# Kernel optimization log

Hardware: AMD Instinct MI355X
Metric: run time of the kernel (lower is better)

## Reference

```python
import jax, jax.numpy as jnp
import numpy as np
import math

D_MODEL = 1024
N_HEAD = 16


def setup_inputs() -> dict:
    key = jax.random.key(0)
    k1, k2, k3 = jax.random.split(key, 3)
    B, S, E = 2, 2048, D_MODEL
    x = jax.random.normal(k1, (B, S, E), dtype=jnp.float32)
    # Linear weights stored as (in, out); init scaled like typical transformer init
    w_attn = jax.random.normal(k2, (E, 3 * E), dtype=jnp.float32) * (1.0 / math.sqrt(E))
    w_proj = jax.random.normal(k3, (E, E), dtype=jnp.float32) * (1.0 / math.sqrt(E))
    return {"x": x, "w_attn": w_attn, "w_proj": w_proj}


def reference(x, w_attn, w_proj):
    B, S, E = x.shape
    H = N_HEAD
    Dh = E // H
    qkv = x @ w_attn  # (B, S, 3E)
    q, k, v = jnp.split(qkv, 3, axis=-1)
    # (B, H, S, Dh)
    q = q.reshape(B, S, H, Dh).transpose(0, 2, 1, 3)
    k = k.reshape(B, S, H, Dh).transpose(0, 2, 1, 3)
    v = v.reshape(B, S, H, Dh).transpose(0, 2, 1, 3)
    scale = 1.0 / math.sqrt(Dh)
    att = jnp.einsum('bhqd,bhkd->bhqk', q, k) * scale  # (B, H, S, S)
    causal = jnp.tril(jnp.ones((S, S), dtype=bool))
    att = jnp.where(causal, att, -jnp.inf)
    att = jax.nn.softmax(att, axis=-1)
    # dropout = 0.0 (eval mode) -> identity
    y = jnp.einsum('bhqk,bhkd->bhqd', att, v)  # (B, H, S, Dh)
    y = y.transpose(0, 2, 1, 3).reshape(B, S, E)
    return y @ w_proj
```

## Files before the change

kernel.cpp:

```cpp
#include <hip/hip_runtime.h>
#include <hip/hip_bf16.h>

#define S_LEN 2048
#define EMB   1024
#define NH    16
#define DH    64
#define QKV_LD 3072

typedef __attribute__((ext_vector_type(8)))  __bf16 bf16x8;
typedef __attribute__((ext_vector_type(4)))  __bf16 bf16x4;
typedef __attribute__((ext_vector_type(4)))  float  f32x4;
typedef __attribute__((ext_vector_type(16))) float  f32x16;
typedef __attribute__((ext_vector_type(2)))  unsigned int u32x2;

__device__ __forceinline__ void gl_lds16(const void* g, void* l) {
  __builtin_amdgcn_global_load_lds(
      (const __attribute__((address_space(1))) void*)g,
      (__attribute__((address_space(3))) void*)l,
      16, 0, 0);
}

__global__ __launch_bounds__(256)
void prep_fused(const float* __restrict__ x, __bf16* __restrict__ xb,
                const float* __restrict__ w_attn, __bf16* __restrict__ wat,
                const float* __restrict__ w_proj, __bf16* __restrict__ wpt,
                int n8) {
  __shared__ float T[64][65];
  const int bid = blockIdx.x;
  const int tid = threadIdx.x;

  if (bid < 2048) {
    int i = bid * 256 + tid;
    if (i >= n8) return;
    const f32x4* p = (const f32x4*)(x + (size_t)i * 8);
    f32x4 a = p[0], b = p[1];
    bf16x8 o;
    #pragma unroll
    for (int j = 0; j < 4; j++) { o[j] = (__bf16)a[j]; o[4 + j] = (__bf16)b[j]; }
    *(bf16x8*)(xb + (size_t)i * 8) = o;
    return;
  }

  const float* W; __bf16* Wt; int K, N, k0, n0;
  if (bid < 2048 + 768) {
    int t = bid - 2048;
    W = w_attn; Wt = wat; K = 1024; N = 3072;
    n0 = (t % 48) * 64; k0 = (t / 48) * 64;
  } else {
    int t = bid - 2816;
    W = w_proj; Wt = wpt; K = 1024; N = 1024;
    n0 = (t & 15) * 64; k0 = (t >> 4) * 64;
  }
  #pragma unroll
  for (int t = 0; t < 16; t++) {
    int idx = tid + t * 256;
    int r = idx >> 6, c = idx & 63;
    T[r][c] = W[(size_t)(k0 + r) * N + n0 + c];
  }
  __syncthreads();
  #pragma unroll
  for (int t = 0; t < 16; t++) {
    int idx = tid + t * 256;
    int r = idx >> 6, c = idx & 63;
    Wt[(size_t)(n0 + r) * K + k0 + c] = (__bf16)T[c][r];
  }
}

#define TM 128
#define TK 32

template <typename OutT, int TNv>
__global__ __launch_bounds__(256, 2)
void gemm_bf16_mfma(const __bf16* __restrict__ A, const __bf16* __restrict__ Bt,
                    OutT* __restrict__ C, int M, int N, int K) {
  __shared__ __align__(16) __bf16 As[2][TM][TK];
  __shared__ __align__(16) __bf16 Bs[2][TNv][TK];
  const int tid  = threadIdx.x;
  const int lane = tid & 63;
  const int w    = tid >> 6;
  const int wr   = w >> 1, wc = w & 1;
  const int brow = blockIdx.y * TM;
  const int bcol = blockIdx.x * TNv;
  const int l15  = lane & 15;
  const int grp  = lane >> 4;

  constexpr int NBI = TNv / 64;
  constexpr int WCT = TNv / 2;
  constexpr int NN  = WCT / 16;

  auto stage = [&](int k0, int buf) {
    #pragma unroll
    for (int j = 0; j < 2; j++) {
      const int cid = w * 128 + j * 64 + lane;
      const int row = cid >> 2, k8 = (cid & 3) * 8;
      gl_lds16(A + (size_t)(brow + row) * K + k0 + k8,
               &As[buf][0][0] + (size_t)(w * 128 + j * 64) * 8);
    }
    #pragma unroll
    for (int j = 0; j < NBI; j++) {
      const int cid = (w * NBI + j) * 64 + lane;
      const int row = cid >> 2, k8 = (cid & 3) * 8;
      gl_lds16(Bt + (size_t)(bcol + row) * K + k0 + k8,
               &Bs[buf][0][0] + (size_t)((w * NBI + j) * 64) * 8);
    }
  };

  f32x4 acc[4][NN];
  #pragma unroll
  for (int m = 0; m < 4; m++)
    #pragma unroll
    for (int n = 0; n < NN; n++) acc[m][n] = (f32x4){0.f, 0.f, 0.f, 0.f};

  stage(0, 0);
  __syncthreads();

  const int nk = K / TK;
  for (int kt = 0; kt < nk; kt++) {
    const int cur = kt & 1;
    if (kt + 1 < nk) stage((kt + 1) * TK, cur ^ 1);

    bf16x8 a[4], b[NN];
    #pragma unroll
    for (int m = 0; m < 4; m++)
      a[m] = *(const bf16x8*)&As[cur][wr * 64 + m * 16 + l15][grp * 8];
    #pragma unroll
    for (int n = 0; n < NN; n++)
      b[n] = *(const bf16x8*)&Bs[cur][wc * WCT + n * 16 + l15][grp * 8];
    #pragma unroll
    for (int m = 0; m < 4; m++)
      #pragma unroll
      for (int n = 0; n < NN; n++)
        acc[m][n] = __builtin_amdgcn_mfma_f32_16x16x32_bf16(a[m], b[n], acc[m][n], 0, 0, 0);

    __syncthreads();
  }

  #pragma unroll
  for (int m = 0; m < 4; m++)
    #pragma unroll
    for (int r = 0; r < 4; r++) {
      const size_t row = (size_t)(brow + wr * 64 + m * 16 + grp * 4 + r);
      #pragma unroll
      for (int n = 0; n < NN; n++)
        C[row * N + bcol + wc * WCT + n * 16 + l15] = (OutT)acc[m][n][r];
    }
}

#define QB 64
#define KB 64
#define QSCALE 0.18033688f

__device__ __constant__ unsigned char ITEMS[44] = {
  76, 72, 68, 64,
  125, 127, 121, 60,
  123, 117, 119, 113, 56,
  115, 109, 111, 105, 52,
  107, 101, 103, 97, 48,
  99, 93, 95, 89, 44,
  91, 85, 87, 81, 40,
  83, 36,
  32, 28, 24, 20, 16, 12, 8, 4, 0
};

__global__ __launch_bounds__(256, 4)
void attn_mfma(const __bf16* __restrict__ qkv, __bf16* __restrict__ y,
               float* __restrict__ pO, float* __restrict__ pml) {
  __shared__ __align__(16) __bf16 Ks[3][KB][64];
  __shared__ __align__(16) __bf16 Vs[3][4096];

  const int tid  = threadIdx.x;
  const int lane = tid & 63;
  const int w    = tid >> 6;

  const int bid = blockIdx.x;
  const int xcd = bid & 7;
  const int j   = bid >> 3;
  const int g   = xcd * 4 + j / 44;
  const int idx = j % 44;

  const int code  = ITEMS[idx];
  const bool split = code & 1;
  const int khalf = (code >> 1) & 1;
  const int qtile = code >> 2;

  int it0, it1;
  bool diag;
  if (!split) {
    it0 = 0; it1 = qtile + 1; diag = true;
  } else {
    const int half = (qtile + 2) >> 1;
    it0 = khalf ? half : 0;
    it1 = khalf ? qtile + 1 : half;
    diag = (khalf == 1);
  }
  const int h = g & 15, b = g >> 4;
  const int pidx = split ? ((g * 12 + (qtile - 20)) * 2 + khalf) : 0;

  const __bf16* base = qkv + (size_t)b * S_LEN * QKV_LD;

  const int l31 = lane & 31;
  const int hl  = lane >> 5;
  const int qh  = w >> 1;
  const int kh  = w & 1;

  const int voff32 = ((lane >> 4) & 1) * 2048 + hl * 128 + (lane & 15) * 8
                   + kh * 1024;

  auto stageK = [&](int j0, int buf) {
    #pragma unroll
    for (int jj = 0; jj < 2; jj++) {
      const int cid = w * 128 + jj * 64 + lane;
      const int r = cid >> 3, pc = cid & 7;
      const int lc = pc ^ (r & 7);
      gl_lds16(base + (size_t)(j0 + r) * QKV_LD + EMB + h * DH + lc * 8,
               (char*)&Ks[buf][0][0] + (w * 128 + jj * 64) * 16);
    }
  };
  auto stageV = [&](int j0, int buf) {
    #pragma unroll
    for (int jj = 0; jj < 2; jj++) {
      const int cid = w * 128 + jj * 64 + lane;
      const int db = cid >> 7, sk = (cid >> 3) & 15;
      const int jr = (cid >> 1) & 3, ch = cid & 1;
      gl_lds16(base + (size_t)(j0 + sk * 4 + jr) * QKV_LD + 2 * EMB + h * DH
                    + db * 16 + ch * 8,
               (char*)&Vs[buf][0] + (w * 128 + jj * 64) * 16);
    }
  };

  const int qbase = qtile * QB;
  const int q = qbase + qh * 32 + l31;

  bf16x8 qf[4];
  {
    const __bf16* qp = base + (size_t)q * QKV_LD + h * DH;
    #pragma unroll
    for (int dq = 0; dq < 4; dq++) {
      bf16x8 v = *(const bf16x8*)(qp + dq * 16 + hl * 8);
      #pragma unroll
      for (int i2 = 0; i2 < 8; i2++) qf[dq][i2] = (__bf16)((float)v[i2] * QSCALE);
    }
  }

  f32x16 o_acc[2];
  #pragma unroll
  for (int d2 = 0; d2 < 2; d2++)
    #pragma unroll
    for (int r = 0; r < 16; r++) o_acc[d2][r] = 0.f;
  float m = -1e30f, l = 0.f;

  auto process = [&](int cur, int j0, bool masked) {
    f32x16 s, s2;
    #pragma unroll
    for (int r = 0; r < 16; r++) { s[r] = 0.f; s2[r] = 0.f; }
    const int krow = kh * 32 + l31;
    bf16x8 kf0 = *(const bf16x8*)&Ks[cur][krow][((0 + hl) ^ (krow & 7)) * 8];
    bf16x8 kf1 = *(const bf16x8*)&Ks[cur][krow][((2 + hl) ^ (krow & 7)) * 8];
    bf16x8 kf2 = *(const bf16x8*)&Ks[cur][krow][((4 + hl) ^ (krow & 7)) * 8];
    bf16x8 kf3 = *(const bf16x8*)&Ks[cur][krow][((6 + hl) ^ (krow & 7)) * 8];
    __builtin_amdgcn_s_setprio(1);
    s  = __builtin_amdgcn_mfma_f32_32x32x16_bf16(kf0, qf[0], s,  0, 0, 0);
    s2 = __builtin_amdgcn_mfma_f32_32x32x16_bf16(kf1, qf[1], s2, 0, 0, 0);
    s  = __builtin_amdgcn_mfma_f32_32x32x16_bf16(kf2, qf[2], s,  0, 0, 0);
    s2 = __builtin_amdgcn_mfma_f32_32x32x16_bf16(kf3, qf[3], s2, 0, 0, 0);
    __builtin_amdgcn_s_setprio(0);

    const unsigned vb =
        (unsigned)(uintptr_t)(__attribute__((address_space(3))) char*)(&Vs[cur][0])
        + (unsigned)voff32;
    u32x2 tv[8];
    asm volatile("ds_read_b64_tr_b16 %0, %1 offset:0"    : "=v"(tv[0]) : "v"(vb));
    asm volatile("ds_read_b64_tr_b16 %0, %1 offset:256"  : "=v"(tv[1]) : "v"(vb));
    asm volatile("ds_read_b64_tr_b16 %0, %1 offset:512"  : "=v"(tv[2]) : "v"(vb));
    asm volatile("ds_read_b64_tr_b16 %0, %1 offset:768"  : "=v"(tv[3]) : "v"(vb));
    asm volatile("ds_read_b64_tr_b16 %0, %1 offset:4096" : "=v"(tv[4]) : "v"(vb));
    asm volatile("ds_read_b64_tr_b16 %0, %1 offset:4352" : "=v"(tv[5]) : "v"(vb));
    asm volatile("ds_read_b64_tr_b16 %0, %1 offset:4608" : "=v"(tv[6]) : "v"(vb));
    asm volatile("ds_read_b64_tr_b16 %0, %1 offset:4864" : "=v"(tv[7]) : "v"(vb));

    #pragma unroll
    for (int r = 0; r < 16; r++) s[r] += s2[r];

    if (masked) {
      const int lim = q - j0 - kh * 32 - 4 * hl;
      #pragma unroll
      for (int r = 0; r < 16; r++) {
        const int kl = (r & 3) + 8 * (r >> 2);
        if (kl > lim) s[r] = -2e30f;
      }
    }

    float x0 = fmaxf(s[0], s[8]),  x1 = fmaxf(s[1], s[9]);
    float x2 = fmaxf(s[2], s[10]), x3 = fmaxf(s[3], s[11]);
    float x4 = fmaxf(s[4], s[12]), x5 = fmaxf(s[5], s[13]);
    float x6 = fmaxf(s[6], s[14]), x7 = fmaxf(s[7], s[15]);
    x0 = fmaxf(x0, x4); x1 = fmaxf(x1, x5);
    x2 = fmaxf(x2, x6); x3 = fmaxf(x3, x7);
    x0 = fmaxf(x0, x2); x1 = fmaxf(x1, x3);
    float tmax = fmaxf(x0, x1);
    tmax = fmaxf(tmax, __shfl_xor(tmax, 32));

    const bool grow = !__all(tmax <= m + 8.0f);
    float corr = 1.f;
    if (grow) {
      const float mnew = fmaxf(m, tmax);
      corr = __builtin_amdgcn_exp2f(m - mnew);
      m = mnew;
    }

    float ps0 = 0.f, ps1 = 0.f, ps2 = 0.f, ps3 = 0.f;
    #pragma unroll
    for (int r = 0; r < 16; r += 4) {
      float p0 = __builtin_amdgcn_exp2f(s[r]     - m);
      float p1 = __builtin_amdgcn_exp2f(s[r + 1] - m);
      float p2 = __builtin_amdgcn_exp2f(s[r + 2] - m);
      float p3 = __builtin_amdgcn_exp2f(s[r + 3] - m);
      s[r] = p0; s[r + 1] = p1; s[r + 2] = p2; s[r + 3] = p3;
      ps0 += p0; ps1 += p1; ps2 += p2; ps3 += p3;
    }
    float psum = (ps0 + ps1) + (ps2 + ps3);

    bf16x8 pb0, pb1;
    #pragma unroll
    for (int i2 = 0; i2 < 8; i2++) {
      pb0[i2] = (__bf16)s[i2];
      pb1[i2] = (__bf16)s[8 + i2];
    }

    if (grow) {
      #pragma unroll
      for (int d2 = 0; d2 < 2; d2++)
        #pragma unroll
        for (int r = 0; r < 16; r++) o_acc[d2][r] *= corr;
    }

    asm volatile("s_waitcnt lgkmcnt(0)");
    __builtin_amdgcn_sched_barrier(0);
    __builtin_amdgcn_s_setprio(1);
    #pragma unroll
    for (int d2 = 0; d2 < 2; d2++) {
      bf16x8 a0, a1;
      ((u32x2*)&a0)[0] = tv[d2 * 4 + 0]; ((u32x2*)&a0)[1] = tv[d2 * 4 + 1];
      ((u32x2*)&a1)[0] = tv[d2 * 4 + 2]; ((u32x2*)&a1)[1] = tv[d2 * 4 + 3];
      o_acc[d2] = __builtin_amdgcn_mfma_f32_32x32x16_bf16(a0, pb0, o_acc[d2], 0, 0, 0);
      o_acc[d2] = __builtin_amdgcn_mfma_f32_32x32x16_bf16(a1, pb1, o_acc[d2], 0, 0, 0);
    }
    __builtin_amdgcn_s_setprio(0);

    psum += __shfl_xor(psum, 32);
    l = grow ? (l * corr + psum) : (l + psum);
  };

  const int nt = it1 - it0;
  stageK(it0 * KB, 0);
  stageV(it0 * KB, 0);
  if (nt > 1) { stageK((it0 + 1) * KB, 1); stageV((it0 + 1) * KB, 1); }

  int cur = 0;
  #pragma unroll 1
  for (int tt = 0; tt < nt; tt++) {
    if (tt < nt - 1) asm volatile("s_waitcnt vmcnt(4)" ::: "memory");
    else             asm volatile("s_waitcnt vmcnt(0)" ::: "memory");
    __builtin_amdgcn_s_barrier();
    __builtin_amdgcn_sched_barrier(0);
    if (tt + 2 < nt) {
      int nb = cur + 2; if (nb >= 3) nb -= 3;
      stageK((it0 + tt + 2) * KB, nb);
      stageV((it0 + tt + 2) * KB, nb);
    }
    process(cur, (it0 + tt) * KB, (tt == nt - 1) && diag);
    cur = (cur == 2) ? 0 : cur + 1;
  }

  __syncthreads();
  float* exO  = (float*)&Vs[0][0];
  float* exML = (float*)&Ks[0][0][0];
  const int slot = qh * 64 + lane;
  if (kh) {
    #pragma unroll
    for (int r = 0; r < 16; r++) {
      exO[r * 128 + slot]        = o_acc[0][r];
      exO[(16 + r) * 128 + slot] = o_acc[1][r];
    }
    exML[slot]       = m;
    exML[128 + slot] = l;
  }
  __syncthreads();
  if (!kh) {
    const float m1  = exML[slot];
    const float l1v = exML[128 + slot];
    const float mm = fmaxf(m, m1);
    const float c0 = __builtin_amdgcn_exp2f(m - mm);
    const float c1 = __builtin_amdgcn_exp2f(m1 - mm);
    const float lsum = l * c0 + l1v * c1;
    if (split) {
      float* prow = pO + (size_t)pidx * 4096 + (size_t)(qh * 32 + l31) * 64;
      #pragma unroll
      for (int d2 = 0; d2 < 2; d2++)
        #pragma unroll
        for (int rq = 0; rq < 4; rq++) {
          f32x4 o4;
          #pragma unroll
          for (int jj = 0; jj < 4; jj++) {
            const int r = rq * 4 + jj;
            o4[jj] = o_acc[d2][r] * c0 + exO[(d2 * 16 + r) * 128 + slot] * c1;
          }
          *(f32x4*)&prow[d2 * 32 + rq * 8 + hl * 4] = o4;
        }
      if (!hl) {
        pml[(size_t)pidx * 128 + qh * 32 + l31]      = mm;
        pml[(size_t)pidx * 128 + 64 + qh * 32 + l31] = lsum;
      }
    } else {
      const float inv = 1.f / lsum;
      __bf16* yrow = y + ((size_t)(b * S_LEN + q)) * EMB + h * DH;
      #pragma unroll
      for (int d2 = 0; d2 < 2; d2++)
        #pragma unroll
        for (int rq = 0; rq < 4; rq++) {
          bf16x4 o4;
          #pragma unroll
          for (int jj = 0; jj < 4; jj++) {
            const int r = rq * 4 + jj;
            float v = (o_acc[d2][r] * c0 + exO[(d2 * 16 + r) * 128 + slot] * c1) * inv;
            o4[jj] = (__bf16)v;
          }
          *(bf16x4*)&yrow[d2 * 32 + rq * 8 + hl * 4] = o4;
        }
    }
  }
}

__global__ __launch_bounds__(256)
void attn_merge(const float* __restrict__ pO, const float* __restrict__ pml,
                __bf16* __restrict__ y) {
  const int mid = blockIdx.x;
  const int g = mid / 12, qrel = mid % 12;
  const int qt = 20 + qrel;
  const int b = g >> 4, h = g & 15;
  const int p0 = (g * 12 + qrel) * 2, p1 = p0 + 1;
  const int row = threadIdx.x >> 2;
  const int d0  = (threadIdx.x & 3) * 16;

  const float mA = pml[(size_t)p0 * 128 + row];
  const float lA = pml[(size_t)p0 * 128 + 64 + row];
  const float mB = pml[(size_t)p1 * 128 + row];
  const float lB = pml[(size_t)p1 * 128 + 64 + row];
  const float mm = fmaxf(mA, mB);
  const float cA = __builtin_amdgcn_exp2f(mA - mm);
  const float cB = __builtin_amdgcn_exp2f(mB - mm);
  const float inv = 1.f / (lA * cA + lB * cB);

  const float* OA = pO + (size_t)p0 * 4096 + (size_t)row * 64 + d0;
  const float* OB = pO + (size_t)p1 * 4096 + (size_t)row * 64 + d0;
  __bf16* yr = y + ((size_t)(b * S_LEN + qt * 64 + row)) * EMB + h * DH + d0;
  #pragma unroll
  for (int i = 0; i < 4; i++) {
    f32x4 va = *(const f32x4*)(OA + i * 4);
    f32x4 vb = *(const f32x4*)(OB + i * 4);
    bf16x4 o;
    #pragma unroll
    for (int jj = 0; jj < 4; jj++)
      o[jj] = (__bf16)((va[jj] * cA + vb[jj] * cB) * inv);
    *(bf16x4*)(yr + i * 4) = o;
  }
}

extern "C" void kernel_launch(void* const* d_in, const int* in_sizes, int n_in,
                              void* d_out, int out_size, void* d_ws, size_t ws_size,
                              hipStream_t stream) {
  const float* x      = (const float*)d_in[0];
  const float* w_attn = (const float*)d_in[1];
  const float* w_proj = (const float*)d_in[2];
  float* out = (float*)d_out;

  const int B = in_sizes[0] / (S_LEN * EMB);
  const int M = B * S_LEN;

  __bf16* xb   = (__bf16*)d_ws;
  __bf16* wat  = xb  + (size_t)M * EMB;
  __bf16* wpt  = wat + (size_t)QKV_LD * EMB;
  __bf16* qkvb = wpt + (size_t)EMB * EMB;
  __bf16* yb   = qkvb + (size_t)M * QKV_LD;

  float* pO  = (float*)d_ws;
  float* pml = pO + (size_t)768 * 4096;

  {
    int n8 = (M * EMB) / 8;
    prep_fused<<<dim3(3072), 256, 0, stream>>>(x, xb, w_attn, wat, w_proj, wpt, n8);
  }

  dim3 g1(QKV_LD / 128, M / TM);
  gemm_bf16_mfma<__bf16, 128><<<g1, 256, 0, stream>>>(xb, wat, qkvb, M, QKV_LD, EMB);

  attn_mfma<<<dim3(1408), 256, 0, stream>>>(qkvb, yb, pO, pml);
  attn_merge<<<dim3(384), 256, 0, stream>>>(pO, pml, yb);

  dim3 g3(EMB / 64, M / TM);
  gemm_bf16_mfma<float, 64><<<g3, 256, 0, stream>>>(yb, wpt, out, M, EMB, EMB);
}
```

Before: 127.0 us.

## Use single-buffered LDS with in-iteration restaging to cut shared memory

Replaces the triple-buffered K/V shared memory ring with one K and one V buffer in a single byte array. The next tile is issued mid-iteration: K is restaged after QK^T and the max are done, and V after the transposed V reads complete, with barriers guarding each reuse. The two-accumulator QK^T split is folded into a single MFMA chain. This shrinks LDS per block, which can allow more resident blocks, but prefetch distance drops from two tiles to roughly half an iteration and each iteration gains extra barriers and a full vmcnt wait, so global-load latency may be exposed.

```diff
diff --git a/kernel.cpp b/kernel.cpp
--- a/kernel.cpp
+++ b/kernel.cpp
@@ -165,8 +165,9 @@
 __global__ __launch_bounds__(256, 4)
 void attn_mfma(const __bf16* __restrict__ qkv, __bf16* __restrict__ y,
                float* __restrict__ pO, float* __restrict__ pml) {
-  __shared__ __align__(16) __bf16 Ks[3][KB][64];
-  __shared__ __align__(16) __bf16 Vs[3][4096];
+  __shared__ __align__(16) char SMEM[17408];
+  __bf16 (*Ks)[64] = (__bf16 (*)[64])SMEM;
+  __bf16* Vs = (__bf16*)(SMEM + 8192);
 
   const int tid  = threadIdx.x;
   const int lane = tid & 63;
@@ -206,17 +207,17 @@
   const int voff32 = ((lane >> 4) & 1) * 2048 + hl * 128 + (lane & 15) * 8
                    + kh * 1024;
 
-  auto stageK = [&](int j0, int buf) {
+  auto stageK = [&](int j0) {
     #pragma unroll
     for (int jj = 0; jj < 2; jj++) {
       const int cid = w * 128 + jj * 64 + lane;
       const int r = cid >> 3, pc = cid & 7;
       const int lc = pc ^ (r & 7);
       gl_lds16(base + (size_t)(j0 + r) * QKV_LD + EMB + h * DH + lc * 8,
-               (char*)&Ks[buf][0][0] + (w * 128 + jj * 64) * 16);
+               SMEM + (w * 128 + jj * 64) * 16);
     }
   };
-  auto stageV = [&](int j0, int buf) {
+  auto stageV = [&](int j0) {
     #pragma unroll
     for (int jj = 0; jj < 2; jj++) {
       const int cid = w * 128 + jj * 64 + lane;
@@ -224,7 +225,7 @@
       const int jr = (cid >> 1) & 3, ch = cid & 1;
       gl_lds16(base + (size_t)(j0 + sk * 4 + jr) * QKV_LD + 2 * EMB + h * DH
                     + db * 16 + ch * 8,
-               (char*)&Vs[buf][0] + (w * 128 + jj * 64) * 16);
+               SMEM + 8192 + (w * 128 + jj * 64) * 16);
     }
   };
 
@@ -249,24 +250,34 @@
     for (int r = 0; r < 16; r++) o_acc[d2][r] = 0.f;
   float m = -1e30f, l = 0.f;
 
-  auto process = [&](int cur, int j0, bool masked) {
-    f32x16 s, s2;
-    #pragma unroll
-    for (int r = 0; r < 16; r++) { s[r] = 0.f; s2[r] = 0.f; }
+  auto iter = [&](int j0, bool masked, int jn, bool do_stage) {
+    asm volatile("s_waitcnt vmcnt(0)" ::: "memory");
+    __builtin_amdgcn_s_barrier();
+    __builtin_amdgcn_sched_barrier(0);
+
+    f32x16 s;
+    #pragma unroll
+    for (int r = 0; r < 16; r++) s[r] = 0.f;
     const int krow = kh * 32 + l31;
-    bf16x8 kf0 = *(const bf16x8*)&Ks[cur][krow][((0 + hl) ^ (krow & 7)) * 8];
-    bf16x8 kf1 = *(const bf16x8*)&Ks[cur][krow][((2 + hl) ^ (krow & 7)) * 8];
-    bf16x8 kf2 = *(const bf16x8*)&Ks[cur][krow][((4 + hl) ^ (krow & 7)) * 8];
-    bf16x8 kf3 = *(const bf16x8*)&Ks[cur][krow][((6 + hl) ^ (krow & 7)) * 8];
     __builtin_amdgcn_s_setprio(1);
-    s  = __builtin_amdgcn_mfma_f32_32x32x16_bf16(kf0, qf[0], s,  0, 0, 0);
-    s2 = __builtin_amdgcn_mfma_f32_32x32x16_bf16(kf1, qf[1], s2, 0, 0, 0);
-    s  = __builtin_amdgcn_mfma_f32_32x32x16_bf16(kf2, qf[2], s,  0, 0, 0);
-    s2 = __builtin_amdgcn_mfma_f32_32x32x16_bf16(kf3, qf[3], s2, 0, 0, 0);
+    #pragma unroll
+    for (int dq = 0; dq < 4; dq++) {
+      bf16x8 kf = *(const bf16x8*)&Ks[krow][((dq * 2 + hl) ^ (krow & 7)) * 8];
+      s = __builtin_amdgcn_mfma_f32_32x32x16_bf16(kf, qf[dq], s, 0, 0, 0);
+    }
     __builtin_amdgcn_s_setprio(0);
 
+    if (masked) {
+      const int lim = q - j0 - kh * 32 - 4 * hl;
+      #pragma unroll
+      for (int r = 0; r < 16; r++) {
+        const int kl = (r & 3) + 8 * (r >> 2);
+        if (kl > lim) s[r] = -2e30f;
+      }
+    }
+
     const unsigned vb =
-        (unsigned)(uintptr_t)(__attribute__((address_space(3))) char*)(&Vs[cur][0])
+        (unsigned)(uintptr_t)(__attribute__((address_space(3))) char*)(Vs)
         + (unsigned)voff32;
     u32x2 tv[8];
     asm volatile("ds_read_b64_tr_b16 %0, %1 offset:0"    : "=v"(tv[0]) : "v"(vb));
@@ -278,18 +289,6 @@
     asm volatile("ds_read_b64_tr_b16 %0, %1 offset:4608" : "=v"(tv[6]) : "v"(vb));
     asm volatile("ds_read_b64_tr_b16 %0, %1 offset:4864" : "=v"(tv[7]) : "v"(vb));
 
-    #pragma unroll
-    for (int r = 0; r < 16; r++) s[r] += s2[r];
-
-    if (masked) {
-      const int lim = q - j0 - kh * 32 - 4 * hl;
-      #pragma unroll
-      for (int r = 0; r < 16; r++) {
-        const int kl = (r & 3) + 8 * (r >> 2);
-        if (kl > lim) s[r] = -2e30f;
-      }
-    }
-
     float x0 = fmaxf(s[0], s[8]),  x1 = fmaxf(s[1], s[9]);
     float x2 = fmaxf(s[2], s[10]), x3 = fmaxf(s[3], s[11]);
     float x4 = fmaxf(s[4], s[12]), x5 = fmaxf(s[5], s[13]);
@@ -308,6 +307,14 @@
       m = mnew;
     }
 
+    __builtin_amdgcn_s_barrier();
+    if (do_stage) stageK(jn);
+
+    asm volatile("s_waitcnt lgkmcnt(0)" ::: "memory");
+    __builtin_amdgcn_sched_barrier(0);
+    __builtin_amdgcn_s_barrier();
+    if (do_stage) stageV(jn);
+
     float ps0 = 0.f, ps1 = 0.f, ps2 = 0.f, ps3 = 0.f;
     #pragma unroll
     for (int r = 0; r < 16; r += 4) {
@@ -334,8 +341,6 @@
         for (int r = 0; r < 16; r++) o_acc[d2][r] *= corr;
     }
 
-    asm volatile("s_waitcnt lgkmcnt(0)");
-    __builtin_amdgcn_sched_barrier(0);
     __builtin_amdgcn_s_setprio(1);
     #pragma unroll
     for (int d2 = 0; d2 < 2; d2++) {
@@ -351,30 +356,19 @@
     l = grow ? (l * corr + psum) : (l + psum);
   };
 
+  stageK(it0 * KB);
+  stageV(it0 * KB);
+
   const int nt = it1 - it0;
-  stageK(it0 * KB, 0);
-  stageV(it0 * KB, 0);
-  if (nt > 1) { stageK((it0 + 1) * KB, 1); stageV((it0 + 1) * KB, 1); }
-
-  int cur = 0;
   #pragma unroll 1
   for (int tt = 0; tt < nt; tt++) {
-    if (tt < nt - 1) asm volatile("s_waitcnt vmcnt(4)" ::: "memory");
-    else             asm volatile("s_waitcnt vmcnt(0)" ::: "memory");
-    __builtin_amdgcn_s_barrier();
-    __builtin_amdgcn_sched_barrier(0);
-    if (tt + 2 < nt) {
-      int nb = cur + 2; if (nb >= 3) nb -= 3;
-      stageK((it0 + tt + 2) * KB, nb);
-      stageV((it0 + tt + 2) * KB, nb);
-    }
-    process(cur, (it0 + tt) * KB, (tt == nt - 1) && diag);
-    cur = (cur == 2) ? 0 : cur + 1;
+    iter((it0 + tt) * KB, (tt == nt - 1) && diag,
+         (it0 + tt + 1) * KB, tt + 1 < nt);
   }
 
   __syncthreads();
-  float* exO  = (float*)&Vs[0][0];
-  float* exML = (float*)&Ks[0][0][0];
+  float* exO  = (float*)SMEM;
+  float* exML = (float*)(SMEM + 16384);
   const int slot = qh * 64 + lane;
   if (kh) {
     #pragma unroll
```

After: 109.6 us. -13.7%, faster.
